# Kernel tuning notes

Hardware: AMD Instinct MI355X
Metric: run time of the kernel (lower is better)

Reference implementation:

```python
import jax, jax.numpy as jnp
import numpy as np

EMBED = 1024
HEADS = 16
HEAD_DIM = EMBED // HEADS


def setup_inputs() -> dict:
    key = jax.random.key(0)
    ks = jax.random.split(key, 7)
    B, Sd, Se = 4, 2048, 2048
    dec = jax.random.normal(ks[0], (B, Sd, EMBED), dtype=jnp.float32)
    enc = jax.random.normal(ks[1], (B, Se, EMBED), dtype=jnp.float32)
    scale = 1.0 / np.sqrt(EMBED)
    W_q = jax.random.normal(ks[2], (EMBED, EMBED), dtype=jnp.float32) * scale
    W_k = jax.random.normal(ks[3], (EMBED, EMBED), dtype=jnp.float32) * scale
    W_v = jax.random.normal(ks[4], (EMBED, EMBED), dtype=jnp.float32) * scale
    W_o = jax.random.normal(ks[5], (EMBED, EMBED), dtype=jnp.float32) * scale
    b_o = jax.random.normal(ks[6], (EMBED,), dtype=jnp.float32) * 0.01
    return {"decoder_input": dec, "encoder_output": enc,
            "W_q": W_q, "W_k": W_k, "W_v": W_v, "W_o": W_o, "b_o": b_o}


def reference(decoder_input, encoder_output, W_q, W_k, W_v, W_o, b_o):
    B, Sd, E = decoder_input.shape
    Se = encoder_output.shape[1]
    # projections (nn.Linear applies x @ W.T; here W is stored as [in, out])
    Q = (decoder_input @ W_q).reshape(B, Sd, HEADS, HEAD_DIM)
    K = (encoder_output @ W_k).reshape(B, Se, HEADS, HEAD_DIM)
    V = (encoder_output @ W_v).reshape(B, Se, HEADS, HEAD_DIM)
    # scores: [B, H, Sd, Se]
    scores = jnp.einsum('bqhd,bkhd->bhqk', Q, K) / jnp.sqrt(jnp.float32(HEAD_DIM))
    attn = jax.nn.softmax(scores, axis=-1)
    out = jnp.einsum('bhqk,bkhd->bqhd', attn, V).reshape(B, Sd, E)
    return out @ W_o + b_o
```

## Files before the change

kernel.cpp:

```cpp
#include <hip/hip_runtime.h>
#include <hip/hip_bf16.h>

namespace {

typedef __attribute__((ext_vector_type(8))) short bf16x8;
typedef __attribute__((ext_vector_type(4))) float f32x4;

constexpr int BATCH = 4;
constexpr int SEQ   = 2048;
constexpr int EMB   = 1024;
constexpr int NH    = 16;
constexpr int HD    = 64;
constexpr int MTOT  = BATCH * SEQ;
constexpr int KVW   = 2 * EMB;
constexpr float LOG2E = 1.44269504088896f;
constexpr float SOFTMAX_C = 16.0f;

__device__ __forceinline__ unsigned short f2bf(float x) {
    unsigned int u = __float_as_uint(x);
    u += 0x7fffu + ((u >> 16) & 1u);
    return (unsigned short)(u >> 16);
}

__device__ __forceinline__ unsigned pack_bf16(float lo, float hi) {
    unsigned ul = __float_as_uint(lo) + 0x8000u;
    unsigned uh = __float_as_uint(hi) + 0x8000u;
    return __builtin_amdgcn_perm(uh, ul, 0x07060302u);
}

__global__ __launch_bounds__(256)
void conv_bf16(const float* __restrict__ dec, const float* __restrict__ enc,
               unsigned short* __restrict__ decb, unsigned short* __restrict__ encb,
               int n4)
{
    int i = blockIdx.x * 256 + threadIdx.x;
    if (i >= n4) return;
    const float* src = blockIdx.y ? enc : dec;
    unsigned short* dst = blockIdx.y ? encb : decb;
    float4 v = ((const float4*)src)[i];
    ushort4 o;
    o.x = f2bf(v.x); o.y = f2bf(v.y); o.z = f2bf(v.z); o.w = f2bf(v.w);
    ((ushort4*)dst)[i] = o;
}

__global__ __launch_bounds__(256)
void wtrans(const float* __restrict__ W0, const float* __restrict__ W1,
            const float* __restrict__ W2, const float* __restrict__ W3,
            unsigned short* __restrict__ WtBase, float qscale)
{
    __shared__ __align__(16) unsigned short Ts[64][65];
    const int tid = threadIdx.x;
    const int z = blockIdx.z;
    const float* W = (z == 0) ? W0 : (z == 1) ? W1 : (z == 2) ? W2 : W3;
    unsigned short* Wt = WtBase + (size_t)z * EMB * EMB;
    const float scale = (z == 0) ? qscale : 1.0f;
    const int n0 = blockIdx.x * 64, k0 = blockIdx.y * 64;
    #pragma unroll
    for (int i = 0; i < 4; ++i) {
        int id = tid + i * 256;
        int r = id >> 4, q = id & 15;
        float4 v = *(const float4*)&W[(size_t)(k0 + r) * EMB + n0 + q * 4];
        Ts[q * 4 + 0][r] = f2bf(v.x * scale);
        Ts[q * 4 + 1][r] = f2bf(v.y * scale);
        Ts[q * 4 + 2][r] = f2bf(v.z * scale);
        Ts[q * 4 + 3][r] = f2bf(v.w * scale);
    }
    __syncthreads();
    #pragma unroll
    for (int i = 0; i < 4; ++i) {
        int id = tid + i * 256;
        int rn = id >> 4, q = id & 15;
        ushort4 o;
        o.x = Ts[rn][q * 4 + 0]; o.y = Ts[rn][q * 4 + 1];
        o.z = Ts[rn][q * 4 + 2]; o.w = Ts[rn][q * 4 + 3];
        *(ushort4*)&Wt[(size_t)(n0 + rn) * EMB + k0 + q * 4] = o;
    }
}

__global__ __launch_bounds__(256)
void vtrans(const unsigned short* __restrict__ V, unsigned short* __restrict__ Vt)
{
    __shared__ __align__(16) unsigned short Ts[64][72];
    const int tid = threadIdx.x;
    const int s0 = blockIdx.x * 64;
    const int bh = blockIdx.y, b = bh >> 4, h = bh & 15;
    #pragma unroll
    for (int it = 0; it < 2; ++it) {
        int id = tid + it * 256;
        int r = id >> 3, seg = id & 7;
        uint4 v = *(const uint4*)&V[(size_t)(b * SEQ + s0 + r) * KVW + h * HD + seg * 8];
        const unsigned short* pv = (const unsigned short*)&v;
        #pragma unroll
        for (int j = 0; j < 8; ++j) Ts[seg * 8 + j][r] = pv[j];
    }
    __syncthreads();
    #pragma unroll
    for (int it = 0; it < 2; ++it) {
        int id = tid + it * 256;
        int d = id >> 3, sg = id & 7;
        uint4 w = *(const uint4*)&Ts[d][sg * 8];
        *(uint4*)&Vt[((size_t)bh * HD + d) * SEQ + s0 + sg * 8] = w;
    }
}

template<bool OUT_BF16, bool BIAS>
__device__ __forceinline__
void gemm_body(const unsigned short* __restrict__ A, const unsigned short* __restrict__ Bt,
               const float* __restrict__ bias, void* __restrict__ Cout,
               int m0, int n0, int N, int Kd)
{
    __shared__ __align__(16) unsigned short As[128 * 32];
    __shared__ __align__(16) unsigned short Bs[128 * 32];
    const int tid  = threadIdx.x;
    const int lane = tid & 63, wave = tid >> 6;
    const int g = lane >> 4, c = lane & 15;
    const int wm = (wave & 1) * 64, wn = (wave >> 1) * 64;

    const int r0 = tid >> 2, s = tid & 3;
    const int sg = s ^ ((r0 + (r0 >> 2)) & 3);
    const unsigned short* ga0 = A  + (size_t)(m0 + r0)      * Kd + sg * 8;
    const unsigned short* ga1 = A  + (size_t)(m0 + r0 + 64) * Kd + sg * 8;
    const unsigned short* gb0 = Bt + (size_t)(n0 + r0)      * Kd + sg * 8;
    const unsigned short* gb1 = Bt + (size_t)(n0 + r0 + 64) * Kd + sg * 8;
    unsigned short* la0 = &As[(size_t)tid * 8];
    unsigned short* la1 = &As[(size_t)(256 + tid) * 8];
    unsigned short* lb0 = &Bs[(size_t)tid * 8];
    unsigned short* lb1 = &Bs[(size_t)(256 + tid) * 8];

    const int cs = (c + (c >> 2)) & 3;

    f32x4 acc[4][4];
    #pragma unroll
    for (int i = 0; i < 4; ++i)
        #pragma unroll
        for (int j = 0; j < 4; ++j) acc[i][j] = (f32x4)0.0f;

    uint4 ra0 = *(const uint4*)ga0, ra1 = *(const uint4*)ga1;
    uint4 rb0 = *(const uint4*)gb0, rb1 = *(const uint4*)gb1;
    ga0 += 32; ga1 += 32; gb0 += 32; gb1 += 32;
    *(uint4*)la0 = ra0; *(uint4*)la1 = ra1;
    *(uint4*)lb0 = rb0; *(uint4*)lb1 = rb1;
    ra0 = *(const uint4*)ga0; ra1 = *(const uint4*)ga1;
    rb0 = *(const uint4*)gb0; rb1 = *(const uint4*)gb1;
    ga0 += 32; ga1 += 32; gb0 += 32; gb1 += 32;
    __syncthreads();

    for (int k0 = 0; k0 < Kd; k0 += 32) {
        bf16x8 af[4], bfr[4];
        #pragma unroll
        for (int mt = 0; mt < 4; ++mt)
            af[mt]  = *(const bf16x8*)&As[(wm + mt * 16 + c) * 32 + (g ^ cs) * 8];
        #pragma unroll
        for (int nt = 0; nt < 4; ++nt)
            bfr[nt] = *(const bf16x8*)&Bs[(wn + nt * 16 + c) * 32 + (g ^ cs) * 8];
        #pragma unroll
        for (int mt = 0; mt < 4; ++mt)
            #pragma unroll
            for (int nt = 0; nt < 4; ++nt)
                acc[mt][nt] = __builtin_amdgcn_mfma_f32_16x16x32_bf16(af[mt], bfr[nt], acc[mt][nt], 0, 0, 0);
        __syncthreads();
        if (k0 + 32 < Kd) {
            *(uint4*)la0 = ra0; *(uint4*)la1 = ra1;
            *(uint4*)lb0 = rb0; *(uint4*)lb1 = rb1;
            if (k0 + 64 < Kd) {
                ra0 = *(const uint4*)ga0; ra1 = *(const uint4*)ga1;
                rb0 = *(const uint4*)gb0; rb1 = *(const uint4*)gb1;
                ga0 += 32; ga1 += 32; gb0 += 32; gb1 += 32;
            }
            __syncthreads();
        }
    }

    #pragma unroll
    for (int mt = 0; mt < 4; ++mt) {
        #pragma unroll
        for (int nt = 0; nt < 4; ++nt) {
            int n = n0 + wn + nt * 16 + c;
            float bv = BIAS ? bias[n] : 0.0f;
            #pragma unroll
            for (int r = 0; r < 4; ++r) {
                int m = m0 + wm + mt * 16 + 4 * g + r;
                float v = acc[mt][nt][r] + bv;
                if (OUT_BF16) ((unsigned short*)Cout)[(size_t)m * N + n] = f2bf(v);
                else          ((float*)Cout)[(size_t)m * N + n] = v;
            }
        }
    }
}

__global__ __launch_bounds__(256)
void proj_fused(const unsigned short* __restrict__ decb, const unsigned short* __restrict__ encb,
                const unsigned short* __restrict__ WtBase,
                unsigned short* __restrict__ Qb, unsigned short* __restrict__ KVb)
{
    const int nt = blockIdx.x;
    const int m0 = blockIdx.y * 128;
    if (nt < 8) {
        gemm_body<true, false>(decb, WtBase, nullptr, Qb, m0, nt * 128, EMB, EMB);
    } else {
        gemm_body<true, false>(encb, WtBase + (size_t)EMB * EMB, nullptr, KVb,
                               m0, (nt - 8) * 128, KVW, EMB);
    }
}

__global__ __launch_bounds__(256)
void proj_out(const unsigned short* __restrict__ Ob, const unsigned short* __restrict__ WoT,
              const float* __restrict__ bo, float* __restrict__ out)
{
    gemm_body<false, true>(Ob, WoT, bo, out, blockIdx.y * 128, blockIdx.x * 128, EMB, EMB);
}

__global__ __launch_bounds__(256, 4)
void attn(const unsigned short* __restrict__ Q, const unsigned short* __restrict__ KV,
          const unsigned short* __restrict__ Vt, unsigned short* __restrict__ O)
{
    __shared__ __align__(16) unsigned short Ks[64 * 64];
    __shared__ __align__(16) unsigned short Vs[64 * 64];
    __shared__ __align__(16) unsigned short Ps[4][32][72];

    const int tid  = threadIdx.x;
    const int lane = tid & 63, wave = tid >> 6;
    const int g = lane >> 4, c = lane & 15, c7 = c & 7;
    const int bh = blockIdx.y, b = bh >> 4, h = bh & 15;
    const int qw = blockIdx.x * 128 + wave * 32;

    const unsigned short* Qp0 = Q + (size_t)(b * SEQ + qw + c) * EMB + h * HD;
    const unsigned short* Qp1 = Qp0 + (size_t)16 * EMB;
    bf16x8 qb[2][2];
    qb[0][0] = *(const bf16x8*)(Qp0 + g * 8);
    qb[0][1] = *(const bf16x8*)(Qp0 + 32 + g * 8);
    qb[1][0] = *(const bf16x8*)(Qp1 + g * 8);
    qb[1][1] = *(const bf16x8*)(Qp1 + 32 + g * 8);

    const int r0 = tid >> 3, s8 = tid & 7;
    const int sg = s8 ^ (r0 & 7);
    const unsigned short* gK0 = KV + ((size_t)b * SEQ + r0) * KVW + h * HD + sg * 8;
    const unsigned short* gK1 = gK0 + (size_t)32 * KVW;
    const unsigned short* gV0 = Vt + (size_t)bh * HD * SEQ + (size_t)r0 * SEQ + sg * 8;
    const unsigned short* gV1 = gV0 + (size_t)32 * SEQ;
    unsigned short* lK0 = &Ks[(size_t)tid * 8];
    unsigned short* lK1 = &Ks[(size_t)(256 + tid) * 8];
    unsigned short* lV0 = &Vs[(size_t)tid * 8];
    unsigned short* lV1 = &Vs[(size_t)(256 + tid) * 8];

    f32x4 oac[2][4];
    #pragma unroll
    for (int bd = 0; bd < 2; ++bd)
        #pragma unroll
        for (int dt = 0; dt < 4; ++dt) oac[bd][dt] = (f32x4)0.0f;
    float lrun[2] = {0.0f, 0.0f};
    const f32x4 minit = {-SOFTMAX_C, -SOFTMAX_C, -SOFTMAX_C, -SOFTMAX_C};

    uint4 rk0 = *(const uint4*)gK0, rk1 = *(const uint4*)gK1;
    uint4 rv0 = *(const uint4*)gV0, rv1 = *(const uint4*)gV1;
    gK0 += (size_t)64 * KVW; gK1 += (size_t)64 * KVW; gV0 += 64; gV1 += 64;
    *(uint4*)lK0 = rk0; *(uint4*)lK1 = rk1;
    *(uint4*)lV0 = rv0; *(uint4*)lV1 = rv1;
    rk0 = *(const uint4*)gK0; rk1 = *(const uint4*)gK1;
    rv0 = *(const uint4*)gV0; rv1 = *(const uint4*)gV1;
    gK0 += (size_t)64 * KVW; gK1 += (size_t)64 * KVW; gV0 += 64; gV1 += 64;
    __syncthreads();

    constexpr int T = SEQ / 64;
    for (int t = 0; t < T; ++t) {
        f32x4 st[2][4];
        #pragma unroll
        for (int kt = 0; kt < 4; ++kt) {
            bf16x8 ka0 = *(const bf16x8*)&Ks[(kt * 16 + c) * 64 + (g ^ c7) * 8];
            bf16x8 ka1 = *(const bf16x8*)&Ks[(kt * 16 + c) * 64 + ((4 + g) ^ c7) * 8];
            #pragma unroll
            for (int bd = 0; bd < 2; ++bd) {
                st[bd][kt] = __builtin_amdgcn_mfma_f32_16x16x32_bf16(ka0, qb[bd][0], minit, 0, 0, 0);
                st[bd][kt] = __builtin_amdgcn_mfma_f32_16x16x32_bf16(ka1, qb[bd][1], st[bd][kt], 0, 0, 0);
            }
        }

        #pragma unroll
        for (int bd = 0; bd < 2; ++bd) {
            float ls = lrun[bd];
            #pragma unroll
            for (int kt = 0; kt < 4; ++kt) {
                float p0 = __builtin_amdgcn_exp2f(st[bd][kt][0]);
                float p1 = __builtin_amdgcn_exp2f(st[bd][kt][1]);
                float p2 = __builtin_amdgcn_exp2f(st[bd][kt][2]);
                float p3 = __builtin_amdgcn_exp2f(st[bd][kt][3]);
                ls += (p0 + p1) + (p2 + p3);
                uint2 u;
                u.x = pack_bf16(p0, p1);
                u.y = pack_bf16(p2, p3);
                *(uint2*)&Ps[wave][bd * 16 + c][kt * 16 + 4 * g] = u;
            }
            lrun[bd] = ls;
        }

        bf16x8 pa[2][2];
        pa[0][0] = *(const bf16x8*)&Ps[wave][c][g * 8];
        pa[0][1] = *(const bf16x8*)&Ps[wave][c][32 + g * 8];
        pa[1][0] = *(const bf16x8*)&Ps[wave][16 + c][g * 8];
        pa[1][1] = *(const bf16x8*)&Ps[wave][16 + c][32 + g * 8];
        #pragma unroll
        for (int dt = 0; dt < 4; ++dt) {
            bf16x8 vb0 = *(const bf16x8*)&Vs[(dt * 16 + c) * 64 + (g ^ c7) * 8];
            bf16x8 vb1 = *(const bf16x8*)&Vs[(dt * 16 + c) * 64 + ((4 + g) ^ c7) * 8];
            #pragma unroll
            for (int bd = 0; bd < 2; ++bd) {
                oac[bd][dt] = __builtin_amdgcn_mfma_f32_16x16x32_bf16(pa[bd][0], vb0, oac[bd][dt], 0, 0, 0);
                oac[bd][dt] = __builtin_amdgcn_mfma_f32_16x16x32_bf16(pa[bd][1], vb1, oac[bd][dt], 0, 0, 0);
            }
        }

        __syncthreads();
        if (t + 1 < T) {
            *(uint4*)lK0 = rk0; *(uint4*)lK1 = rk1;
            *(uint4*)lV0 = rv0; *(uint4*)lV1 = rv1;
            if (t + 2 < T) {
                rk0 = *(const uint4*)gK0; rk1 = *(const uint4*)gK1;
                rv0 = *(const uint4*)gV0; rv1 = *(const uint4*)gV1;
                gK0 += (size_t)64 * KVW; gK1 += (size_t)64 * KVW;
                gV0 += 64;               gV1 += 64;
            }
            __syncthreads();
        }
    }

    #pragma unroll
    for (int bd = 0; bd < 2; ++bd) {
        float v = lrun[bd];
        v += __shfl_xor(v, 16);
        v += __shfl_xor(v, 32);
        lrun[bd] = v;
    }
    #pragma unroll
    for (int bd = 0; bd < 2; ++bd) {
        unsigned short* Op = O + (size_t)(b * SEQ + qw + bd * 16) * EMB + h * HD;
        #pragma unroll
        for (int r = 0; r < 4; ++r) {
            float linv = 1.0f / __shfl(lrun[bd], 4 * g + r);
            #pragma unroll
            for (int dt = 0; dt < 4; ++dt)
                Op[(size_t)(4 * g + r) * EMB + dt * 16 + c] = f2bf(oac[bd][dt][r] * linv);
        }
    }
}

}

extern "C" void kernel_launch(void* const* d_in, const int* in_sizes, int n_in,
                              void* d_out, int out_size, void* d_ws, size_t ws_size,
                              hipStream_t stream)
{
    const float* dec = (const float*)d_in[0];
    const float* enc = (const float*)d_in[1];
    const float* Wq  = (const float*)d_in[2];
    const float* Wk  = (const float*)d_in[3];
    const float* Wv  = (const float*)d_in[4];
    const float* Wo  = (const float*)d_in[5];
    const float* bo  = (const float*)d_in[6];
    float* out = (float*)d_out;

    const size_t BIG = (size_t)MTOT * EMB;
    const size_t SML = (size_t)EMB * EMB;
    unsigned short* decb = (unsigned short*)d_ws;
    unsigned short* encb = decb + BIG;
    unsigned short* WqT  = encb + BIG;
    unsigned short* WoT  = WqT + 3 * SML;
    unsigned short* Qb   = WqT + 4 * SML;
    unsigned short* KVb  = Qb + BIG;
    unsigned short* Vtg  = KVb + 2 * BIG;
    unsigned short* Ob   = Vtg + BIG;

    dim3 blk(256);

    conv_bf16<<<dim3((unsigned)(BIG / 4 / 256), 2), blk, 0, stream>>>(
        dec, enc, decb, encb, (int)(BIG / 4));

    wtrans<<<dim3(16, 16, 4), blk, 0, stream>>>(Wq, Wk, Wv, Wo, WqT, 0.125f * LOG2E);

    proj_fused<<<dim3(24, MTOT / 128), blk, 0, stream>>>(decb, encb, WqT, Qb, KVb);

    vtrans<<<dim3(SEQ / 64, BATCH * NH), blk, 0, stream>>>(KVb + EMB, Vtg);

    attn<<<dim3(SEQ / 128, BATCH * NH), blk, 0, stream>>>(Qb, KVb, Vtg, Ob);

    proj_out<<<dim3(EMB / 128, MTOT / 128), blk, 0, stream>>>(Ob, WoT, bo, out);
}
```

Measured before the change: 357.5 us.

## Use direct global-to-LDS loads with double-buffered shared tiles in GEMM and attention

Replaces the register-staged global loads followed by LDS stores with global_load_lds direct copies into double-buffered shared memory, in both the GEMM body and the attention kernel. The next tile is prefetched into the other buffer while the current one is consumed, and each step now needs one barrier instead of two. This aims to cut VGPR pressure and hide load latency. In exchange, the attention LDS footprint doubles for K/V and its occupancy hint in launch_bounds is dropped, which may lower the number of resident blocks.

```diff
diff --git a/kernel.cpp b/kernel.cpp
--- a/kernel.cpp
+++ b/kernel.cpp
@@ -28,6 +28,12 @@
     return __builtin_amdgcn_perm(uh, ul, 0x07060302u);
 }
 
+__device__ __forceinline__ void gl_lds16(const void* g, void* l) {
+    __builtin_amdgcn_global_load_lds(
+        (const __attribute__((address_space(1))) unsigned int*)g,
+        (__attribute__((address_space(3))) unsigned int*)l, 16, 0, 0);
+}
+
 __global__ __launch_bounds__(256)
 void conv_bf16(const float* __restrict__ dec, const float* __restrict__ enc,
                unsigned short* __restrict__ decb, unsigned short* __restrict__ encb,
@@ -109,8 +115,8 @@
                const float* __restrict__ bias, void* __restrict__ Cout,
                int m0, int n0, int N, int Kd)
 {
-    __shared__ __align__(16) unsigned short As[128 * 32];
-    __shared__ __align__(16) unsigned short Bs[128 * 32];
+    __shared__ __align__(16) unsigned short As[2][128 * 32];
+    __shared__ __align__(16) unsigned short Bs[2][128 * 32];
     const int tid  = threadIdx.x;
     const int lane = tid & 63, wave = tid >> 6;
     const int g = lane >> 4, c = lane & 15;
@@ -122,10 +128,7 @@
     const unsigned short* ga1 = A  + (size_t)(m0 + r0 + 64) * Kd + sg * 8;
     const unsigned short* gb0 = Bt + (size_t)(n0 + r0)      * Kd + sg * 8;
     const unsigned short* gb1 = Bt + (size_t)(n0 + r0 + 64) * Kd + sg * 8;
-    unsigned short* la0 = &As[(size_t)tid * 8];
-    unsigned short* la1 = &As[(size_t)(256 + tid) * 8];
-    unsigned short* lb0 = &Bs[(size_t)tid * 8];
-    unsigned short* lb1 = &Bs[(size_t)(256 + tid) * 8];
+    const int lo0 = tid * 8, lo1 = (256 + tid) * 8;
 
     const int cs = (c + (c >> 2)) & 3;
 
@@ -135,38 +138,33 @@
         #pragma unroll
         for (int j = 0; j < 4; ++j) acc[i][j] = (f32x4)0.0f;
 
-    uint4 ra0 = *(const uint4*)ga0, ra1 = *(const uint4*)ga1;
-    uint4 rb0 = *(const uint4*)gb0, rb1 = *(const uint4*)gb1;
-    ga0 += 32; ga1 += 32; gb0 += 32; gb1 += 32;
-    *(uint4*)la0 = ra0; *(uint4*)la1 = ra1;
-    *(uint4*)lb0 = rb0; *(uint4*)lb1 = rb1;
-    ra0 = *(const uint4*)ga0; ra1 = *(const uint4*)ga1;
-    rb0 = *(const uint4*)gb0; rb1 = *(const uint4*)gb1;
+    gl_lds16(ga0, &As[0][lo0]); gl_lds16(ga1, &As[0][lo1]);
+    gl_lds16(gb0, &Bs[0][lo0]); gl_lds16(gb1, &Bs[0][lo1]);
     ga0 += 32; ga1 += 32; gb0 += 32; gb1 += 32;
     __syncthreads();
 
-    for (int k0 = 0; k0 < Kd; k0 += 32) {
-        bf16x8 af[4], bfr[4];
-        #pragma unroll
-        for (int mt = 0; mt < 4; ++mt)
-            af[mt]  = *(const bf16x8*)&As[(wm + mt * 16 + c) * 32 + (g ^ cs) * 8];
-        #pragma unroll
-        for (int nt = 0; nt < 4; ++nt)
-            bfr[nt] = *(const bf16x8*)&Bs[(wn + nt * 16 + c) * 32 + (g ^ cs) * 8];
-        #pragma unroll
-        for (int mt = 0; mt < 4; ++mt)
+    const int KT = Kd / 32;
+    for (int kt = 0; kt < KT; kt += 2) {
+        #pragma unroll
+        for (int h2 = 0; h2 < 2; ++h2) {
+            const int k = kt + h2;
+            if (k + 1 < KT) {
+                gl_lds16(ga0, &As[h2 ^ 1][lo0]); gl_lds16(ga1, &As[h2 ^ 1][lo1]);
+                gl_lds16(gb0, &Bs[h2 ^ 1][lo0]); gl_lds16(gb1, &Bs[h2 ^ 1][lo1]);
+                ga0 += 32; ga1 += 32; gb0 += 32; gb1 += 32;
+            }
+            bf16x8 af[4], bfr[4];
+            #pragma unroll
+            for (int mt = 0; mt < 4; ++mt)
+                af[mt]  = *(const bf16x8*)&As[h2][(wm + mt * 16 + c) * 32 + (g ^ cs) * 8];
             #pragma unroll
             for (int nt = 0; nt < 4; ++nt)
-                acc[mt][nt] = __builtin_amdgcn_mfma_f32_16x16x32_bf16(af[mt], bfr[nt], acc[mt][nt], 0, 0, 0);
-        __syncthreads();
-        if (k0 + 32 < Kd) {
-            *(uint4*)la0 = ra0; *(uint4*)la1 = ra1;
-            *(uint4*)lb0 = rb0; *(uint4*)lb1 = rb1;
-            if (k0 + 64 < Kd) {
-                ra0 = *(const uint4*)ga0; ra1 = *(const uint4*)ga1;
-                rb0 = *(const uint4*)gb0; rb1 = *(const uint4*)gb1;
-                ga0 += 32; ga1 += 32; gb0 += 32; gb1 += 32;
-            }
+                bfr[nt] = *(const bf16x8*)&Bs[h2][(wn + nt * 16 + c) * 32 + (g ^ cs) * 8];
+            #pragma unroll
+            for (int mt = 0; mt < 4; ++mt)
+                #pragma unroll
+                for (int nt = 0; nt < 4; ++nt)
+                    acc[mt][nt] = __builtin_amdgcn_mfma_f32_16x16x32_bf16(af[mt], bfr[nt], acc[mt][nt], 0, 0, 0);
             __syncthreads();
         }
     }
@@ -210,12 +208,12 @@
     gemm_body<false, true>(Ob, WoT, bo, out, blockIdx.y * 128, blockIdx.x * 128, EMB, EMB);
 }
 
-__global__ __launch_bounds__(256, 4)
+__global__ __launch_bounds__(256)
 void attn(const unsigned short* __restrict__ Q, const unsigned short* __restrict__ KV,
           const unsigned short* __restrict__ Vt, unsigned short* __restrict__ O)
 {
-    __shared__ __align__(16) unsigned short Ks[64 * 64];
-    __shared__ __align__(16) unsigned short Vs[64 * 64];
+    __shared__ __align__(16) unsigned short Ks[2][64 * 64];
+    __shared__ __align__(16) unsigned short Vs[2][64 * 64];
     __shared__ __align__(16) unsigned short Ps[4][32][72];
 
     const int tid  = threadIdx.x;
@@ -238,10 +236,7 @@
     const unsigned short* gK1 = gK0 + (size_t)32 * KVW;
     const unsigned short* gV0 = Vt + (size_t)bh * HD * SEQ + (size_t)r0 * SEQ + sg * 8;
     const unsigned short* gV1 = gV0 + (size_t)32 * SEQ;
-    unsigned short* lK0 = &Ks[(size_t)tid * 8];
-    unsigned short* lK1 = &Ks[(size_t)(256 + tid) * 8];
-    unsigned short* lV0 = &Vs[(size_t)tid * 8];
-    unsigned short* lV1 = &Vs[(size_t)(256 + tid) * 8];
+    const int lo0 = tid * 8, lo1 = (256 + tid) * 8;
 
     f32x4 oac[2][4];
     #pragma unroll
@@ -251,74 +246,69 @@
     float lrun[2] = {0.0f, 0.0f};
     const f32x4 minit = {-SOFTMAX_C, -SOFTMAX_C, -SOFTMAX_C, -SOFTMAX_C};
 
-    uint4 rk0 = *(const uint4*)gK0, rk1 = *(const uint4*)gK1;
-    uint4 rv0 = *(const uint4*)gV0, rv1 = *(const uint4*)gV1;
-    gK0 += (size_t)64 * KVW; gK1 += (size_t)64 * KVW; gV0 += 64; gV1 += 64;
-    *(uint4*)lK0 = rk0; *(uint4*)lK1 = rk1;
-    *(uint4*)lV0 = rv0; *(uint4*)lV1 = rv1;
-    rk0 = *(const uint4*)gK0; rk1 = *(const uint4*)gK1;
-    rv0 = *(const uint4*)gV0; rv1 = *(const uint4*)gV1;
+    gl_lds16(gK0, &Ks[0][lo0]); gl_lds16(gK1, &Ks[0][lo1]);
+    gl_lds16(gV0, &Vs[0][lo0]); gl_lds16(gV1, &Vs[0][lo1]);
     gK0 += (size_t)64 * KVW; gK1 += (size_t)64 * KVW; gV0 += 64; gV1 += 64;
     __syncthreads();
 
     constexpr int T = SEQ / 64;
-    for (int t = 0; t < T; ++t) {
-        f32x4 st[2][4];
-        #pragma unroll
-        for (int kt = 0; kt < 4; ++kt) {
-            bf16x8 ka0 = *(const bf16x8*)&Ks[(kt * 16 + c) * 64 + (g ^ c7) * 8];
-            bf16x8 ka1 = *(const bf16x8*)&Ks[(kt * 16 + c) * 64 + ((4 + g) ^ c7) * 8];
-            #pragma unroll
-            for (int bd = 0; bd < 2; ++bd) {
-                st[bd][kt] = __builtin_amdgcn_mfma_f32_16x16x32_bf16(ka0, qb[bd][0], minit, 0, 0, 0);
-                st[bd][kt] = __builtin_amdgcn_mfma_f32_16x16x32_bf16(ka1, qb[bd][1], st[bd][kt], 0, 0, 0);
-            }
-        }
-
-        #pragma unroll
-        for (int bd = 0; bd < 2; ++bd) {
-            float ls = lrun[bd];
-            #pragma unroll
-            for (int kt = 0; kt < 4; ++kt) {
-                float p0 = __builtin_amdgcn_exp2f(st[bd][kt][0]);
-                float p1 = __builtin_amdgcn_exp2f(st[bd][kt][1]);
-                float p2 = __builtin_amdgcn_exp2f(st[bd][kt][2]);
-                float p3 = __builtin_amdgcn_exp2f(st[bd][kt][3]);
-                ls += (p0 + p1) + (p2 + p3);
-                uint2 u;
-                u.x = pack_bf16(p0, p1);
-                u.y = pack_bf16(p2, p3);
-                *(uint2*)&Ps[wave][bd * 16 + c][kt * 16 + 4 * g] = u;
-            }
-            lrun[bd] = ls;
-        }
-
-        bf16x8 pa[2][2];
-        pa[0][0] = *(const bf16x8*)&Ps[wave][c][g * 8];
-        pa[0][1] = *(const bf16x8*)&Ps[wave][c][32 + g * 8];
-        pa[1][0] = *(const bf16x8*)&Ps[wave][16 + c][g * 8];
-        pa[1][1] = *(const bf16x8*)&Ps[wave][16 + c][32 + g * 8];
-        #pragma unroll
-        for (int dt = 0; dt < 4; ++dt) {
-            bf16x8 vb0 = *(const bf16x8*)&Vs[(dt * 16 + c) * 64 + (g ^ c7) * 8];
-            bf16x8 vb1 = *(const bf16x8*)&Vs[(dt * 16 + c) * 64 + ((4 + g) ^ c7) * 8];
-            #pragma unroll
-            for (int bd = 0; bd < 2; ++bd) {
-                oac[bd][dt] = __builtin_amdgcn_mfma_f32_16x16x32_bf16(pa[bd][0], vb0, oac[bd][dt], 0, 0, 0);
-                oac[bd][dt] = __builtin_amdgcn_mfma_f32_16x16x32_bf16(pa[bd][1], vb1, oac[bd][dt], 0, 0, 0);
-            }
-        }
-
-        __syncthreads();
-        if (t + 1 < T) {
-            *(uint4*)lK0 = rk0; *(uint4*)lK1 = rk1;
-            *(uint4*)lV0 = rv0; *(uint4*)lV1 = rv1;
-            if (t + 2 < T) {
-                rk0 = *(const uint4*)gK0; rk1 = *(const uint4*)gK1;
-                rv0 = *(const uint4*)gV0; rv1 = *(const uint4*)gV1;
+    for (int t = 0; t < T; t += 2) {
+        #pragma unroll
+        for (int h2 = 0; h2 < 2; ++h2) {
+            const int tt = t + h2;
+            if (tt + 1 < T) {
+                gl_lds16(gK0, &Ks[h2 ^ 1][lo0]); gl_lds16(gK1, &Ks[h2 ^ 1][lo1]);
+                gl_lds16(gV0, &Vs[h2 ^ 1][lo0]); gl_lds16(gV1, &Vs[h2 ^ 1][lo1]);
                 gK0 += (size_t)64 * KVW; gK1 += (size_t)64 * KVW;
                 gV0 += 64;               gV1 += 64;
             }
+
+            f32x4 st[2][4];
+            #pragma unroll
+            for (int kt = 0; kt < 4; ++kt) {
+                bf16x8 ka0 = *(const bf16x8*)&Ks[h2][(kt * 16 + c) * 64 + (g ^ c7) * 8];
+                bf16x8 ka1 = *(const bf16x8*)&Ks[h2][(kt * 16 + c) * 64 + ((4 + g) ^ c7) * 8];
+                #pragma unroll
+                for (int bd = 0; bd < 2; ++bd) {
+                    st[bd][kt] = __builtin_amdgcn_mfma_f32_16x16x32_bf16(ka0, qb[bd][0], minit, 0, 0, 0);
+                    st[bd][kt] = __builtin_amdgcn_mfma_f32_16x16x32_bf16(ka1, qb[bd][1], st[bd][kt], 0, 0, 0);
+                }
+            }
+
+            #pragma unroll
+            for (int bd = 0; bd < 2; ++bd) {
+                float ls = lrun[bd];
+                #pragma unroll
+                for (int kt = 0; kt < 4; ++kt) {
+                    float p0 = __builtin_amdgcn_exp2f(st[bd][kt][0]);
+                    float p1 = __builtin_amdgcn_exp2f(st[bd][kt][1]);
+                    float p2 = __builtin_amdgcn_exp2f(st[bd][kt][2]);
+                    float p3 = __builtin_amdgcn_exp2f(st[bd][kt][3]);
+                    ls += (p0 + p1) + (p2 + p3);
+                    uint2 u;
+                    u.x = pack_bf16(p0, p1);
+                    u.y = pack_bf16(p2, p3);
+                    *(uint2*)&Ps[wave][bd * 16 + c][kt * 16 + 4 * g] = u;
+                }
+                lrun[bd] = ls;
+            }
+
+            bf16x8 pa[2][2];
+            pa[0][0] = *(const bf16x8*)&Ps[wave][c][g * 8];
+            pa[0][1] = *(const bf16x8*)&Ps[wave][c][32 + g * 8];
+            pa[1][0] = *(const bf16x8*)&Ps[wave][16 + c][g * 8];
+            pa[1][1] = *(const bf16x8*)&Ps[wave][16 + c][32 + g * 8];
+            #pragma unroll
+            for (int dt = 0; dt < 4; ++dt) {
+                bf16x8 vb0 = *(const bf16x8*)&Vs[h2][(dt * 16 + c) * 64 + (g ^ c7) * 8];
+                bf16x8 vb1 = *(const bf16x8*)&Vs[h2][(dt * 16 + c) * 64 + ((4 + g) ^ c7) * 8];
+                #pragma unroll
+                for (int bd = 0; bd < 2; ++bd) {
+                    oac[bd][dt] = __builtin_amdgcn_mfma_f32_16x16x32_bf16(pa[bd][0], vb0, oac[bd][dt], 0, 0, 0);
+                    oac[bd][dt] = __builtin_amdgcn_mfma_f32_16x16x32_bf16(pa[bd][1], vb1, oac[bd][dt], 0, 0, 0);
+                }
+            }
+
             __syncthreads();
         }
     }
```

Measured after the change: 334.8 us. 1.07x faster.
